# Performance work log

Hardware: AMD Instinct MI355X
Metric: run time of the kernel (lower is better)

The kernel has to match this reference:

```python
import jax, jax.numpy as jnp
import numpy as np

N = 4096      # nodes
INS = 256     # input feature dim
OUTS = 64     # per-mechanism output dim
M = 4         # N_mechs
LEAK = 0.2    # leaky relu negative slope
NEG_INF = -1e9


def setup_inputs() -> dict:
    key = jax.random.key(0)
    ks = jax.random.split(key, 7)
    x = jax.random.normal(ks[0], (N, INS), dtype=jnp.float32)
    adj = jax.random.randint(ks[1], (N, N), 0, 2).astype(jnp.int32)
    W = jax.random.normal(ks[2], (M, INS, OUTS), dtype=jnp.float32) * 0.1
    a1 = jax.random.normal(ks[3], (M, OUTS), dtype=jnp.float32) * 0.1
    a2 = jax.random.normal(ks[4], (M, OUTS), dtype=jnp.float32) * 0.1
    Wc = jax.random.normal(ks[5], (INS, 2 * M * OUTS), dtype=jnp.float32) * 0.1
    bc = jnp.zeros((2 * M * OUTS,), dtype=jnp.float32)
    return {"x": x, "adj": adj, "W": W, "a1": a1, "a2": a2, "Wc": Wc, "bc": bc}


def reference(x, adj, W, a1, a2, Wc, bc):
    # conditioner: mean-pool nodes -> linear -> (gamma, beta) per mechanism
    pooled = x.mean(axis=0)                                   # [INS]
    gb = (pooled @ Wc + bc).reshape(2, M, OUTS)
    gamma, beta = gb[0], gb[1]                                # [M, OUTS] each

    # per-mechanism linear transform + FiLM modulation
    h = jnp.einsum('ni,mio->mno', x, W)                       # [M, N, OUTS]
    h = gamma[:, None, :] * h + beta[:, None, :]

    # GAT-style decomposed attention logits: e_ij = leaky_relu(a1.h_i + a2.h_j)
    e_src = jnp.einsum('mno,mo->mn', h, a1)                   # [M, N]
    e_dst = jnp.einsum('mno,mo->mn', h, a2)                   # [M, N]
    e = e_src[:, :, None] + e_dst[:, None, :]                 # [M, N, N]
    e = jnp.where(e > 0, e, LEAK * e)                         # leaky relu

    # mask by adjacency, softmax over neighbors
    e = jnp.where(adj[None] > 0, e, jnp.float32(NEG_INF))
    attn = jax.nn.softmax(e, axis=-1)                         # [M, N, N]

    out = jnp.einsum('mnk,mko->mno', attn, h)                 # [M, N, OUTS]
    out = jnp.transpose(out, (1, 0, 2)).reshape(N, M * OUTS)  # concat dim=1
    return jax.nn.elu(out)                                    # activate=True
```

## Files before the change

kernel.cpp:

```cpp
#include <hip/hip_runtime.h>
#include <hip/hip_bf16.h>

#define NN    4096
#define INS_  256
#define OUTS_ 64
#define MM    4
#define LOG2E 1.4426950408889634f

typedef float f32x4 __attribute__((ext_vector_type(4)));
typedef short s16x8 __attribute__((ext_vector_type(8)));
typedef unsigned int u32x4 __attribute__((ext_vector_type(4)));

typedef const __attribute__((address_space(1))) unsigned char glob_u8;
typedef __attribute__((address_space(3))) unsigned char lds_u8;

__device__ __forceinline__ void stage16(const void* g, void* l) {
    __builtin_amdgcn_global_load_lds((glob_u8*)g, (lds_u8*)l, 16, 0, 0);
}

__device__ __forceinline__ unsigned int cvt_pk_bf16(float a, float b) {
    unsigned int r;
    asm("v_cvt_pk_bf16_f32 %0, %1, %2" : "=v"(r) : "v"(a), "v"(b));
    return r;
}

__device__ __forceinline__ unsigned int pack_bf16(float a, float b) {
    unsigned int ua = __builtin_bit_cast(unsigned int, a);
    unsigned int ub = __builtin_bit_cast(unsigned int, b);
    ua = (ua + 0x7FFFu + ((ua >> 16) & 1u)) >> 16;
    ub = (ub + 0x7FFFu + ((ub >> 16) & 1u)) & 0xFFFF0000u;
    return ua | ub;
}

__device__ __forceinline__ float mand(float w, unsigned mb, int e) {
    const int m = ((int)(mb << (31 - e))) >> 31;
    return __builtin_bit_cast(float, (__builtin_bit_cast(int, w) & m));
}

__device__ __forceinline__ s16x8 mk_af(float c, unsigned mb,
        const f32x4 q0, const f32x4 q1, const f32x4 q2, const f32x4 q3, float& z) {
    const float w0 = mand(fmaxf(q0[0], c * q0[1]), mb, 0);
    const float w1 = mand(fmaxf(q0[2], c * q0[3]), mb, 1);
    const float w2 = mand(fmaxf(q1[0], c * q1[1]), mb, 2);
    const float w3 = mand(fmaxf(q1[2], c * q1[3]), mb, 3);
    const float w4 = mand(fmaxf(q2[0], c * q2[1]), mb, 4);
    const float w5 = mand(fmaxf(q2[2], c * q2[3]), mb, 5);
    const float w6 = mand(fmaxf(q3[0], c * q3[1]), mb, 6);
    const float w7 = mand(fmaxf(q3[2], c * q3[3]), mb, 7);
    z += ((w0 + w1) + (w2 + w3)) + ((w4 + w5) + (w6 + w7));
    u32x4 au;
    au.x = cvt_pk_bf16(w0, w1);
    au.y = cvt_pk_bf16(w2, w3);
    au.z = cvt_pk_bf16(w4, w5);
    au.w = cvt_pk_bf16(w6, w7);
    return __builtin_bit_cast(s16x8, au);
}


__global__ __launch_bounds__(256) void k_prep(const int* __restrict__ adj,
                                              unsigned long long* __restrict__ msk,
                                              const float* __restrict__ x,
                                              float* __restrict__ part) {
    const int b = blockIdx.x;
    if (b < 1024) {
        const int lane = threadIdx.x & 63;
        const int w    = threadIdx.x >> 6;
        const int r    = b * 4 + w;
        const int* __restrict__ row = adj + (size_t)r * NN;
        unsigned long long* mrow = msk + (size_t)r * 64;
        #pragma unroll 1
        for (int c0 = 0; c0 < 64; c0 += 16) {
            int a[16];
            #pragma unroll
            for (int k = 0; k < 16; ++k) a[k] = row[(c0 + k) * 64 + lane];
            unsigned long long m[16];
            #pragma unroll
            for (int k = 0; k < 16; ++k) m[k] = __ballot(a[k] != 0);
            if (lane == 0) {
                #pragma unroll
                for (int k = 0; k < 16; ++k) mrow[c0 + k] = m[k];
            }
        }
    } else {
        const int bb = b - 1024;
        const int t  = threadIdx.x;
        const int r0 = bb * 64;
        float s = 0.f;
        #pragma unroll 8
        for (int r = 0; r < 64; ++r) s += x[(size_t)(r0 + r) * INS_ + t];
        part[bb * INS_ + t] = s;
    }
}

__global__ __launch_bounds__(256, 2) void k_filmc(
    const float* __restrict__ x, const float* __restrict__ W,
    const float* __restrict__ a1, const float* __restrict__ a2,
    const float* __restrict__ part, const float* __restrict__ Wc,
    const float* __restrict__ bc, float* __restrict__ sc,
    float* __restrict__ spq, unsigned char* __restrict__ htb)
{
    __shared__ float wlds[INS_ * OUTS_];
    __shared__ float sp[INS_];
    __shared__ float pg[256];
    __shared__ float gg[64], bbv[64];

    const int t  = threadIdx.x;
    const int o  = t & 63;
    const int wv = __builtin_amdgcn_readfirstlane(t >> 6);
    const int m  = blockIdx.y;
    const int n0 = blockIdx.x * 32 + wv * 8;

    {
        const unsigned char* wsrc = (const unsigned char*)W + (size_t)m * 65536 + t * 16;
        unsigned char* wdst = (unsigned char*)wlds + t * 16;
        #pragma unroll
        for (int it = 0; it < 16; ++it)
            stage16(wsrc + it * 4096, wdst + it * 4096);
    }

    {
        float s = 0.f;
        #pragma unroll 8
        for (int b = 0; b < 64; ++b) s += part[b * INS_ + t];
        sp[t] = s * (1.0f / NN);
    }
    __syncthreads();

    {
        const int half = t >> 7;
        const int idx  = t & 127;
        const int col  = m * 64 + (idx & 63) + ((idx & 64) ? 256 : 0);
        float acc = (half == 0) ? bc[col] : 0.f;
        const int ib = half * 128;
        #pragma unroll 8
        for (int i = 0; i < 128; ++i)
            acc = fmaf(sp[ib + i], Wc[(size_t)(ib + i) * 512 + col], acc);
        pg[t] = acc;
    }
    __syncthreads();
    if (t < 128) {
        const float v = pg[t] + pg[t + 128];
        if (t < 64) gg[t] = v; else bbv[t - 64] = v;
    }
    __syncthreads();

    float acc[8];
    #pragma unroll
    for (int k = 0; k < 8; ++k) acc[k] = 0.f;

    const float* xp = x + (size_t)n0 * INS_;

    #pragma unroll 4
    for (int i = 0; i < INS_; ++i) {
        const float wl = wlds[i * 64 + o];
        #pragma unroll
        for (int k = 0; k < 8; ++k)
            acc[k] = fmaf(xp[k * INS_ + i], wl, acc[k]);
    }

    const float ga  = gg[o];
    const float be  = bbv[o];
    const float va1 = a1[m * 64 + o];
    const float va2 = a2[m * 64 + o];

    float h[8], sv[8], dv[8];
    #pragma unroll
    for (int k = 0; k < 8; ++k) h[k] = fmaf(ga, acc[k], be);

    #pragma unroll
    for (int k = 0; k < 8; ++k) {
        float s1 = h[k] * va1;
        float s2 = h[k] * va2;
        #pragma unroll
        for (int off = 1; off < 64; off <<= 1) {
            s1 += __shfl_xor(s1, off);
            s2 += __shfl_xor(s2, off);
        }
        sv[k] = s1; dv[k] = s2;
    }

    u32x4 upk;
    upk.x = pack_bf16(h[0], h[1]);
    upk.y = pack_bf16(h[2], h[3]);
    upk.z = pack_bf16(h[4], h[5]);
    upk.w = pack_bf16(h[6], h[7]);
    const size_t phys = ((size_t)(m * 128 + blockIdx.x)) * 4096 + o * 64 + wv * 16;
    *reinterpret_cast<u32x4*>(htb + phys) = upk;

    const int lk = o & 7;
    float ssel = sv[0], dsel = dv[0];
    #pragma unroll
    for (int k = 1; k < 8; ++k) {
        if (lk == k) { ssel = sv[k]; dsel = dv[k]; }
    }
    if (o < 8) {
        sc[(size_t)m * NN + n0 + lk] = exp2f(-0.8f * LOG2E * ssel);
    } else if (o < 16) {
        const float spv = dsel * LOG2E;
        float2 ex = make_float2(exp2f(spv), exp2f(0.2f * spv));
        *reinterpret_cast<float2*>(&spq[(size_t)(m * NN + n0 + lk) * 2]) = ex;
    }
}

#define LOADT(tn, B) do {                                                  \
    const unsigned char* tb_ = tb0 + (size_t)(tn) * 4096;                  \
    B[0] = *reinterpret_cast<const s16x8*>(tb_);                           \
    B[1] = *reinterpret_cast<const s16x8*>(tb_ + 1024);                    \
    B[2] = *reinterpret_cast<const s16x8*>(tb_ + 2048);                    \
    B[3] = *reinterpret_cast<const s16x8*>(tb_ + 3072);                    \
} while (0)

#define COMPUTE4(tn, B, w0_, w1_, w2_, w3_) do {                           \
    const float* qp_ = pqb + (tn) * 64;                                    \
    const f32x4 q0_ = *reinterpret_cast<const f32x4*>(qp_);                \
    const f32x4 q1_ = *reinterpret_cast<const f32x4*>(qp_ + 4);            \
    const f32x4 q2_ = *reinterpret_cast<const f32x4*>(qp_ + 8);            \
    const f32x4 q3_ = *reinterpret_cast<const f32x4*>(qp_ + 12);           \
    const s16x8 A0_ = mk_af(c0v, (w0_) >> sh, q0_, q1_, q2_, q3_, z0);     \
    const s16x8 A1_ = mk_af(c1v, (w1_) >> sh, q0_, q1_, q2_, q3_, z1);     \
    const s16x8 A2_ = mk_af(c2v, (w2_) >> sh, q0_, q1_, q2_, q3_, z2);     \
    const s16x8 A3_ = mk_af(c3v, (w3_) >> sh, q0_, q1_, q2_, q3_, z3);     \
    acc0[0] = __builtin_amdgcn_mfma_f32_16x16x32_bf16(A0_, B[0], acc0[0], 0, 0, 0); \
    acc0[1] = __builtin_amdgcn_mfma_f32_16x16x32_bf16(A0_, B[1], acc0[1], 0, 0, 0); \
    acc0[2] = __builtin_amdgcn_mfma_f32_16x16x32_bf16(A0_, B[2], acc0[2], 0, 0, 0); \
    acc0[3] = __builtin_amdgcn_mfma_f32_16x16x32_bf16(A0_, B[3], acc0[3], 0, 0, 0); \
    acc1[0] = __builtin_amdgcn_mfma_f32_16x16x32_bf16(A1_, B[0], acc1[0], 0, 0, 0); \
    acc1[1] = __builtin_amdgcn_mfma_f32_16x16x32_bf16(A1_, B[1], acc1[1], 0, 0, 0); \
    acc1[2] = __builtin_amdgcn_mfma_f32_16x16x32_bf16(A1_, B[2], acc1[2], 0, 0, 0); \
    acc1[3] = __builtin_amdgcn_mfma_f32_16x16x32_bf16(A1_, B[3], acc1[3], 0, 0, 0); \
    acc2[0] = __builtin_amdgcn_mfma_f32_16x16x32_bf16(A2_, B[0], acc2[0], 0, 0, 0); \
    acc2[1] = __builtin_amdgcn_mfma_f32_16x16x32_bf16(A2_, B[1], acc2[1], 0, 0, 0); \
    acc2[2] = __builtin_amdgcn_mfma_f32_16x16x32_bf16(A2_, B[2], acc2[2], 0, 0, 0); \
    acc2[3] = __builtin_amdgcn_mfma_f32_16x16x32_bf16(A2_, B[3], acc2[3], 0, 0, 0); \
    acc3[0] = __builtin_amdgcn_mfma_f32_16x16x32_bf16(A3_, B[0], acc3[0], 0, 0, 0); \
    acc3[1] = __builtin_amdgcn_mfma_f32_16x16x32_bf16(A3_, B[1], acc3[1], 0, 0, 0); \
    acc3[2] = __builtin_amdgcn_mfma_f32_16x16x32_bf16(A3_, B[2], acc3[2], 0, 0, 0); \
    acc3[3] = __builtin_amdgcn_mfma_f32_16x16x32_bf16(A3_, B[3], acc3[3], 0, 0, 0); \
} while (0)

__global__ __launch_bounds__(512, 2) void k_attn(
    const unsigned int* __restrict__ msk, const float* __restrict__ sc,
    const float* __restrict__ spq, const unsigned char* __restrict__ htb,
    float* __restrict__ out)
{
    extern __shared__ float lds[];
    float* accP = lds;
    float* zP   = lds + 4 * 4096;

    const int t    = threadIdx.x;
    const int lane = t & 63;
    const int jq   = __builtin_amdgcn_readfirstlane(t >> 6);
    const int col  = lane & 15;
    const int kg   = lane >> 4;
    const int sh   = kg * 8;
    const int i0   = blockIdx.x * 64;
    const int mech = blockIdx.y;

    const float c0v = sc[(size_t)mech * NN + i0 + col];
    const float c1v = sc[(size_t)mech * NN + i0 + 16 + col];
    const float c2v = sc[(size_t)mech * NN + i0 + 32 + col];
    const float c3v = sc[(size_t)mech * NN + i0 + 48 + col];

    const u32x4* mr0 = reinterpret_cast<const u32x4*>(
        msk + (size_t)(i0 + col) * 128 + jq * 16);
    const u32x4* mr1 = reinterpret_cast<const u32x4*>(
        msk + (size_t)(i0 + 16 + col) * 128 + jq * 16);
    const u32x4* mr2 = reinterpret_cast<const u32x4*>(
        msk + (size_t)(i0 + 32 + col) * 128 + jq * 16);
    const u32x4* mr3 = reinterpret_cast<const u32x4*>(
        msk + (size_t)(i0 + 48 + col) * 128 + jq * 16);
    const float* pqb = spq + (size_t)mech * NN * 2 + (jq * 512 + kg * 8) * 2;
    const unsigned char* tb0 = htb + ((size_t)(mech * 128 + jq * 16)) * 4096
                             + col * 64 + kg * 16;

    f32x4 acc0[4], acc1[4], acc2[4], acc3[4];
    #pragma unroll
    for (int f = 0; f < 4; ++f) {
        acc0[f] = (f32x4){0.f, 0.f, 0.f, 0.f};
        acc1[f] = acc0[f]; acc2[f] = acc0[f]; acc3[f] = acc0[f];
    }
    float z0 = 0.f, z1 = 0.f, z2 = 0.f, z3 = 0.f;

    s16x8 Ba[4], Bb[4];
    LOADT(0, Ba);
    u32x4 m0n = mr0[0], m1n = mr1[0], m2n = mr2[0], m3n = mr3[0];

    #pragma unroll 1
    for (int tq = 0; tq < 4; ++tq) {
        const int base = tq * 4;
        const u32x4 m0 = m0n, m1 = m1n, m2 = m2n, m3 = m3n;
        if (tq < 3) { m0n = mr0[tq + 1]; m1n = mr1[tq + 1];
                      m2n = mr2[tq + 1]; m3n = mr3[tq + 1]; }
        LOADT(base + 1, Bb);
        COMPUTE4(base + 0, Ba, m0[0], m1[0], m2[0], m3[0]);
        LOADT(base + 2, Ba);
        COMPUTE4(base + 1, Bb, m0[1], m1[1], m2[1], m3[1]);
        LOADT(base + 3, Bb);
        COMPUTE4(base + 2, Ba, m0[2], m1[2], m2[2], m3[2]);
        if (tq < 3) LOADT(base + 4, Ba);
        COMPUTE4(base + 3, Bb, m0[3], m1[3], m2[3], m3[3]);
    }

    z0 += __shfl_xor(z0, 16); z0 += __shfl_xor(z0, 32);
    z1 += __shfl_xor(z1, 16); z1 += __shfl_xor(z1, 32);
    z2 += __shfl_xor(z2, 16); z2 += __shfl_xor(z2, 32);
    z3 += __shfl_xor(z3, 16); z3 += __shfl_xor(z3, 32);

    if (lane < 16) {
        zP[jq * 64 +      lane] = z0;
        zP[jq * 64 + 16 + lane] = z1;
        zP[jq * 64 + 32 + lane] = z2;
        zP[jq * 64 + 48 + lane] = z3;
    }
    float* my = accP + (jq & 3) * 4096;
    if (jq < 4) {
        #pragma unroll
        for (int f = 0; f < 4; ++f) {
            #pragma unroll
            for (int rr = 0; rr < 4; ++rr) {
                const int ro = (kg * 4 + rr) * 64 + f * 16 + col;
                my[ro]            = acc0[f][rr];
                my[1024 + ro]     = acc1[f][rr];
                my[2048 + ro]     = acc2[f][rr];
                my[3072 + ro]     = acc3[f][rr];
            }
        }
    }
    __syncthreads();
    if (jq >= 4) {
        #pragma unroll
        for (int f = 0; f < 4; ++f) {
            #pragma unroll
            for (int rr = 0; rr < 4; ++rr) {
                const int ro = (kg * 4 + rr) * 64 + f * 16 + col;
                my[ro]        += acc0[f][rr];
                my[1024 + ro] += acc1[f][rr];
                my[2048 + ro] += acc2[f][rr];
                my[3072 + ro] += acc3[f][rr];
            }
        }
    }
    __syncthreads();

    const int f0  = t * 8;
    const int row = f0 >> 6;
    const int o0  = f0 & 63;
    f32x4 s0 = (f32x4){0.f, 0.f, 0.f, 0.f};
    f32x4 s1 = s0;
    float z = 0.f;
    #pragma unroll
    for (int p = 0; p < 4; ++p) {
        s0 += *reinterpret_cast<const f32x4*>(accP + p * 4096 + f0);
        s1 += *reinterpret_cast<const f32x4*>(accP + p * 4096 + f0 + 4);
    }
    #pragma unroll
    for (int q = 0; q < 8; ++q) z += zP[q * 64 + row];
    const float inv = 1.0f / z;
    float res[8];
    #pragma unroll
    for (int e = 0; e < 4; ++e) {
        const float v0 = s0[e] * inv;
        const float v1 = s1[e] * inv;
        res[e]     = v0 > 0.f ? v0 : expm1f(v0);
        res[e + 4] = v1 > 0.f ? v1 : expm1f(v1);
    }
    float* op = out + (size_t)(i0 + row) * 256 + mech * 64 + o0;
    *reinterpret_cast<float4*>(op)     = make_float4(res[0], res[1], res[2], res[3]);
    *reinterpret_cast<float4*>(op + 4) = make_float4(res[4], res[5], res[6], res[7]);
}

extern "C" void kernel_launch(void* const* d_in, const int* in_sizes, int n_in,
                              void* d_out, int out_size, void* d_ws, size_t ws_size,
                              hipStream_t stream) {
    const float* x   = (const float*)d_in[0];
    const int*   adj = (const int*)d_in[1];
    const float* W   = (const float*)d_in[2];
    const float* a1  = (const float*)d_in[3];
    const float* a2  = (const float*)d_in[4];
    const float* Wc  = (const float*)d_in[5];
    const float* bc  = (const float*)d_in[6];
    float* out = (float*)d_out;

    float* wsf    = (float*)d_ws;
    float* part   = wsf;
    float* scv    = wsf + 16896;
    float* spq    = wsf + 33280;
    unsigned char* htb = (unsigned char*)(wsf + 66048);
    unsigned long long* msk = (unsigned long long*)(htb + (size_t)2097152);

    (void)hipFuncSetAttribute((const void*)k_attn,
                              hipFuncAttributeMaxDynamicSharedMemorySize, 67584);

    k_prep<<<1088, 256, 0, stream>>>(adj, msk, x, part);
    k_filmc<<<dim3(128, 4), 256, 0, stream>>>(x, W, a1, a2, part, Wc, bc, scv, spq, htb);
    k_attn<<<dim3(64, 4), 512, 67584, stream>>>((const unsigned int*)msk, scv, spq, htb, out);
}
```

Measured before the change: 73.31 us.

## Split attention neighbor range across 16 waves per block instead of 8

Doubles the attention block to 1024 threads so each wave handles half as many neighbor tiles. Wave partial accumulators are then reduced through LDS in four serialized phases, and the z partial sums now come from 16 waves. This targets latency hiding and per-wave serial work in a grid of only 256 blocks. The cost is more LDS reduction passes and barriers, a launch bound of one block per CU that may tighten register limits, and slightly more LDS.

```diff
diff --git a/kernel.cpp b/kernel.cpp
--- a/kernel.cpp
+++ b/kernel.cpp
@@ -238,7 +238,7 @@
     acc3[3] = __builtin_amdgcn_mfma_f32_16x16x32_bf16(A3_, B[3], acc3[3], 0, 0, 0); \
 } while (0)
 
-__global__ __launch_bounds__(512, 2) void k_attn(
+__global__ __launch_bounds__(1024, 1) void k_attn(
     const unsigned int* __restrict__ msk, const float* __restrict__ sc,
     const float* __restrict__ spq, const unsigned char* __restrict__ htb,
     float* __restrict__ out)
@@ -262,15 +262,15 @@
     const float c3v = sc[(size_t)mech * NN + i0 + 48 + col];
 
     const u32x4* mr0 = reinterpret_cast<const u32x4*>(
-        msk + (size_t)(i0 + col) * 128 + jq * 16);
+        msk + (size_t)(i0 + col) * 128 + jq * 8);
     const u32x4* mr1 = reinterpret_cast<const u32x4*>(
-        msk + (size_t)(i0 + 16 + col) * 128 + jq * 16);
+        msk + (size_t)(i0 + 16 + col) * 128 + jq * 8);
     const u32x4* mr2 = reinterpret_cast<const u32x4*>(
-        msk + (size_t)(i0 + 32 + col) * 128 + jq * 16);
+        msk + (size_t)(i0 + 32 + col) * 128 + jq * 8);
     const u32x4* mr3 = reinterpret_cast<const u32x4*>(
-        msk + (size_t)(i0 + 48 + col) * 128 + jq * 16);
-    const float* pqb = spq + (size_t)mech * NN * 2 + (jq * 512 + kg * 8) * 2;
-    const unsigned char* tb0 = htb + ((size_t)(mech * 128 + jq * 16)) * 4096
+        msk + (size_t)(i0 + 48 + col) * 128 + jq * 8);
+    const float* pqb = spq + (size_t)mech * NN * 2 + (jq * 256 + kg * 8) * 2;
+    const unsigned char* tb0 = htb + ((size_t)(mech * 128 + jq * 8)) * 4096
                              + col * 64 + kg * 16;
 
     f32x4 acc0[4], acc1[4], acc2[4], acc3[4];
@@ -286,10 +286,10 @@
     u32x4 m0n = mr0[0], m1n = mr1[0], m2n = mr2[0], m3n = mr3[0];
 
     #pragma unroll 1
-    for (int tq = 0; tq < 4; ++tq) {
+    for (int tq = 0; tq < 2; ++tq) {
         const int base = tq * 4;
         const u32x4 m0 = m0n, m1 = m1n, m2 = m2n, m3 = m3n;
-        if (tq < 3) { m0n = mr0[tq + 1]; m1n = mr1[tq + 1];
+        if (tq < 1) { m0n = mr0[tq + 1]; m1n = mr1[tq + 1];
                       m2n = mr2[tq + 1]; m3n = mr3[tq + 1]; }
         LOADT(base + 1, Bb);
         COMPUTE4(base + 0, Ba, m0[0], m1[0], m2[0], m3[0]);
@@ -297,7 +297,7 @@
         COMPUTE4(base + 1, Bb, m0[1], m1[1], m2[1], m3[1]);
         LOADT(base + 3, Bb);
         COMPUTE4(base + 2, Ba, m0[2], m1[2], m2[2], m3[2]);
-        if (tq < 3) LOADT(base + 4, Ba);
+        if (tq < 1) LOADT(base + 4, Ba);
         COMPUTE4(base + 3, Bb, m0[3], m1[3], m2[3], m3[3]);
     }
 
@@ -313,60 +313,50 @@
         zP[jq * 64 + 48 + lane] = z3;
     }
     float* my = accP + (jq & 3) * 4096;
-    if (jq < 4) {
-        #pragma unroll
-        for (int f = 0; f < 4; ++f) {
+    const int ph = jq >> 2;
+    #pragma unroll 1
+    for (int p = 0; p < 4; ++p) {
+        if (ph == p) {
             #pragma unroll
-            for (int rr = 0; rr < 4; ++rr) {
-                const int ro = (kg * 4 + rr) * 64 + f * 16 + col;
-                my[ro]            = acc0[f][rr];
-                my[1024 + ro]     = acc1[f][rr];
-                my[2048 + ro]     = acc2[f][rr];
-                my[3072 + ro]     = acc3[f][rr];
+            for (int f = 0; f < 4; ++f) {
+                #pragma unroll
+                for (int rr = 0; rr < 4; ++rr) {
+                    const int ro = (kg * 4 + rr) * 64 + f * 16 + col;
+                    if (p == 0) {
+                        my[ro]        = acc0[f][rr];
+                        my[1024 + ro] = acc1[f][rr];
+                        my[2048 + ro] = acc2[f][rr];
+                        my[3072 + ro] = acc3[f][rr];
+                    } else {
+                        my[ro]        += acc0[f][rr];
+                        my[1024 + ro] += acc1[f][rr];
+                        my[2048 + ro] += acc2[f][rr];
+                        my[3072 + ro] += acc3[f][rr];
+                    }
+                }
             }
         }
-    }
-    __syncthreads();
-    if (jq >= 4) {
-        #pragma unroll
-        for (int f = 0; f < 4; ++f) {
-            #pragma unroll
-            for (int rr = 0; rr < 4; ++rr) {
-                const int ro = (kg * 4 + rr) * 64 + f * 16 + col;
-                my[ro]        += acc0[f][rr];
-                my[1024 + ro] += acc1[f][rr];
-                my[2048 + ro] += acc2[f][rr];
-                my[3072 + ro] += acc3[f][rr];
-            }
-        }
-    }
-    __syncthreads();
-
-    const int f0  = t * 8;
+        __syncthreads();
+    }
+
+    const int f0  = t * 4;
     const int row = f0 >> 6;
     const int o0  = f0 & 63;
-    f32x4 s0 = (f32x4){0.f, 0.f, 0.f, 0.f};
-    f32x4 s1 = s0;
+    f32x4 s = (f32x4){0.f, 0.f, 0.f, 0.f};
+    #pragma unroll
+    for (int p = 0; p < 4; ++p)
+        s += *reinterpret_cast<const f32x4*>(accP + p * 4096 + f0);
     float z = 0.f;
     #pragma unroll
-    for (int p = 0; p < 4; ++p) {
-        s0 += *reinterpret_cast<const f32x4*>(accP + p * 4096 + f0);
-        s1 += *reinterpret_cast<const f32x4*>(accP + p * 4096 + f0 + 4);
-    }
-    #pragma unroll
-    for (int q = 0; q < 8; ++q) z += zP[q * 64 + row];
+    for (int q = 0; q < 16; ++q) z += zP[q * 64 + row];
     const float inv = 1.0f / z;
-    float res[8];
+    f32x4 res;
     #pragma unroll
     for (int e = 0; e < 4; ++e) {
-        const float v0 = s0[e] * inv;
-        const float v1 = s1[e] * inv;
-        res[e]     = v0 > 0.f ? v0 : expm1f(v0);
-        res[e + 4] = v1 > 0.f ? v1 : expm1f(v1);
-    }
-    float* op = out + (size_t)(i0 + row) * 256 + mech * 64 + o0;
-    *reinterpret_cast<float4*>(op)     = make_float4(res[0], res[1], res[2], res[3]);
-    *reinterpret_cast<float4*>(op + 4) = make_float4(res[4], res[5], res[6], res[7]);
+        const float v = s[e] * inv;
+        res[e] = v > 0.f ? v : expm1f(v);
+    }
+    *reinterpret_cast<f32x4*>(out + (size_t)(i0 + row) * 256 + mech * 64 + o0) = res;
 }
 
 extern "C" void kernel_launch(void* const* d_in, const int* in_sizes, int n_in,
@@ -389,9 +379,9 @@
     unsigned long long* msk = (unsigned long long*)(htb + (size_t)2097152);
 
     (void)hipFuncSetAttribute((const void*)k_attn,
-                              hipFuncAttributeMaxDynamicSharedMemorySize, 67584);
+                              hipFuncAttributeMaxDynamicSharedMemorySize, 69632);
 
     k_prep<<<1088, 256, 0, stream>>>(adj, msk, x, part);
     k_filmc<<<dim3(128, 4), 256, 0, stream>>>(x, W, a1, a2, part, Wc, bc, scv, spq, htb);
-    k_attn<<<dim3(64, 4), 512, 67584, stream>>>((const unsigned int*)msk, scv, spq, htb, out);
-}
+    k_attn<<<dim3(64, 4), 1024, 69632, stream>>>((const unsigned int*)msk, scv, spq, htb, out);
+}
```

Result: slower. 229.4 us (+212.9%).

## Split attention neighbor dimension across two blocks with last-block reduction

Applied to the files above, without the earlier changes.

Splits k_attn's neighbor (j) range into two halves via a third grid dimension, doubling the block count from 256 to 512 so that more CUs are occupied on the 256-CU part. Each half writes its partial accumulators and softmax denominators to global workspace. The second block to finish, detected with an atomic counter that k_prep zeroes, combines both halves and applies normalization and ELU. In exchange it adds global partial writes and reads, threadfences, and an atomic per output tile.

```diff
diff --git a/kernel.cpp b/kernel.cpp
--- a/kernel.cpp
+++ b/kernel.cpp
@@ -60,7 +60,8 @@
 __global__ __launch_bounds__(256) void k_prep(const int* __restrict__ adj,
                                               unsigned long long* __restrict__ msk,
                                               const float* __restrict__ x,
-                                              float* __restrict__ part) {
+                                              float* __restrict__ part,
+                                              int* __restrict__ cnt) {
     const int b = blockIdx.x;
     if (b < 1024) {
         const int lane = threadIdx.x & 63;
@@ -81,7 +82,7 @@
                 for (int k = 0; k < 16; ++k) mrow[c0 + k] = m[k];
             }
         }
-    } else {
+    } else if (b < 1088) {
         const int bb = b - 1024;
         const int t  = threadIdx.x;
         const int r0 = bb * 64;
@@ -89,6 +90,8 @@
         #pragma unroll 8
         for (int r = 0; r < 64; ++r) s += x[(size_t)(r0 + r) * INS_ + t];
         part[bb * INS_ + t] = s;
+    } else {
+        cnt[threadIdx.x] = 0;
     }
 }
 
@@ -241,11 +244,13 @@
 __global__ __launch_bounds__(512, 2) void k_attn(
     const unsigned int* __restrict__ msk, const float* __restrict__ sc,
     const float* __restrict__ spq, const unsigned char* __restrict__ htb,
-    float* __restrict__ out)
+    float* __restrict__ pacc, float* __restrict__ pz,
+    int* __restrict__ cnt, float* __restrict__ out)
 {
     extern __shared__ float lds[];
     float* accP = lds;
     float* zP   = lds + 4 * 4096;
+    __shared__ int lastFlag;
 
     const int t    = threadIdx.x;
     const int lane = t & 63;
@@ -255,22 +260,24 @@
     const int sh   = kg * 8;
     const int i0   = blockIdx.x * 64;
     const int mech = blockIdx.y;
+    const int jh   = blockIdx.z;
 
     const float c0v = sc[(size_t)mech * NN + i0 + col];
     const float c1v = sc[(size_t)mech * NN + i0 + 16 + col];
     const float c2v = sc[(size_t)mech * NN + i0 + 32 + col];
     const float c3v = sc[(size_t)mech * NN + i0 + 48 + col];
 
+    const int jw = jh * 64 + jq * 8;
     const u32x4* mr0 = reinterpret_cast<const u32x4*>(
-        msk + (size_t)(i0 + col) * 128 + jq * 16);
+        msk + (size_t)(i0 + col) * 128 + jw);
     const u32x4* mr1 = reinterpret_cast<const u32x4*>(
-        msk + (size_t)(i0 + 16 + col) * 128 + jq * 16);
+        msk + (size_t)(i0 + 16 + col) * 128 + jw);
     const u32x4* mr2 = reinterpret_cast<const u32x4*>(
-        msk + (size_t)(i0 + 32 + col) * 128 + jq * 16);
+        msk + (size_t)(i0 + 32 + col) * 128 + jw);
     const u32x4* mr3 = reinterpret_cast<const u32x4*>(
-        msk + (size_t)(i0 + 48 + col) * 128 + jq * 16);
-    const float* pqb = spq + (size_t)mech * NN * 2 + (jq * 512 + kg * 8) * 2;
-    const unsigned char* tb0 = htb + ((size_t)(mech * 128 + jq * 16)) * 4096
+        msk + (size_t)(i0 + 48 + col) * 128 + jw);
+    const float* pqb = spq + (size_t)mech * NN * 2 + ((jh * 2048 + jq * 256) + kg * 8) * 2;
+    const unsigned char* tb0 = htb + ((size_t)(mech * 128 + jh * 64 + jq * 8)) * 4096
                              + col * 64 + kg * 16;
 
     f32x4 acc0[4], acc1[4], acc2[4], acc3[4];
@@ -286,18 +293,17 @@
     u32x4 m0n = mr0[0], m1n = mr1[0], m2n = mr2[0], m3n = mr3[0];
 
     #pragma unroll 1
-    for (int tq = 0; tq < 4; ++tq) {
+    for (int tq = 0; tq < 2; ++tq) {
         const int base = tq * 4;
         const u32x4 m0 = m0n, m1 = m1n, m2 = m2n, m3 = m3n;
-        if (tq < 3) { m0n = mr0[tq + 1]; m1n = mr1[tq + 1];
-                      m2n = mr2[tq + 1]; m3n = mr3[tq + 1]; }
+        if (tq < 1) { m0n = mr0[1]; m1n = mr1[1]; m2n = mr2[1]; m3n = mr3[1]; }
         LOADT(base + 1, Bb);
         COMPUTE4(base + 0, Ba, m0[0], m1[0], m2[0], m3[0]);
         LOADT(base + 2, Ba);
         COMPUTE4(base + 1, Bb, m0[1], m1[1], m2[1], m3[1]);
         LOADT(base + 3, Bb);
         COMPUTE4(base + 2, Ba, m0[2], m1[2], m2[2], m3[2]);
-        if (tq < 3) LOADT(base + 4, Ba);
+        if (tq < 1) LOADT(base + 4, Ba);
         COMPUTE4(base + 3, Bb, m0[3], m1[3], m2[3], m3[3]);
     }
 
@@ -319,10 +325,10 @@
             #pragma unroll
             for (int rr = 0; rr < 4; ++rr) {
                 const int ro = (kg * 4 + rr) * 64 + f * 16 + col;
-                my[ro]            = acc0[f][rr];
-                my[1024 + ro]     = acc1[f][rr];
-                my[2048 + ro]     = acc2[f][rr];
-                my[3072 + ro]     = acc3[f][rr];
+                my[ro]        = acc0[f][rr];
+                my[1024 + ro] = acc1[f][rr];
+                my[2048 + ro] = acc2[f][rr];
+                my[3072 + ro] = acc3[f][rr];
             }
         }
     }
@@ -342,31 +348,52 @@
     }
     __syncthreads();
 
-    const int f0  = t * 8;
-    const int row = f0 >> 6;
-    const int o0  = f0 & 63;
+    const int pair = blockIdx.x * 4 + mech;
+    const int f0   = t * 8;
+    const int row  = f0 >> 6;
     f32x4 s0 = (f32x4){0.f, 0.f, 0.f, 0.f};
     f32x4 s1 = s0;
-    float z = 0.f;
     #pragma unroll
     for (int p = 0; p < 4; ++p) {
         s0 += *reinterpret_cast<const f32x4*>(accP + p * 4096 + f0);
         s1 += *reinterpret_cast<const f32x4*>(accP + p * 4096 + f0 + 4);
     }
-    #pragma unroll
-    for (int q = 0; q < 8; ++q) z += zP[q * 64 + row];
-    const float inv = 1.0f / z;
-    float res[8];
-    #pragma unroll
-    for (int e = 0; e < 4; ++e) {
-        const float v0 = s0[e] * inv;
-        const float v1 = s1[e] * inv;
-        res[e]     = v0 > 0.f ? v0 : expm1f(v0);
-        res[e + 4] = v1 > 0.f ? v1 : expm1f(v1);
-    }
-    float* op = out + (size_t)(i0 + row) * 256 + mech * 64 + o0;
-    *reinterpret_cast<float4*>(op)     = make_float4(res[0], res[1], res[2], res[3]);
-    *reinterpret_cast<float4*>(op + 4) = make_float4(res[4], res[5], res[6], res[7]);
+    float* pa = pacc + ((size_t)(pair * 2 + jh)) * 4096;
+    *reinterpret_cast<f32x4*>(pa + f0)     = s0;
+    *reinterpret_cast<f32x4*>(pa + f0 + 4) = s1;
+    if (t < 64) {
+        float zz = 0.f;
+        #pragma unroll
+        for (int q = 0; q < 8; ++q) zz += zP[q * 64 + t];
+        pz[(pair * 2 + jh) * 64 + t] = zz;
+    }
+    __threadfence();
+    __syncthreads();
+    if (t == 0) lastFlag = atomicAdd(&cnt[pair], 1);
+    __syncthreads();
+
+    if (lastFlag == 1) {
+        __threadfence();
+        const float* paA = pacc + (size_t)pair * 8192;
+        const float* paB = paA + 4096;
+        const f32x4 a0 = *reinterpret_cast<const f32x4*>(paA + f0)
+                       + *reinterpret_cast<const f32x4*>(paB + f0);
+        const f32x4 a1 = *reinterpret_cast<const f32x4*>(paA + f0 + 4)
+                       + *reinterpret_cast<const f32x4*>(paB + f0 + 4);
+        const float z  = pz[pair * 128 + row] + pz[pair * 128 + 64 + row];
+        const float inv = 1.0f / z;
+        float res[8];
+        #pragma unroll
+        for (int e = 0; e < 4; ++e) {
+            const float v0 = a0[e] * inv;
+            const float v1 = a1[e] * inv;
+            res[e]     = v0 > 0.f ? v0 : expm1f(v0);
+            res[e + 4] = v1 > 0.f ? v1 : expm1f(v1);
+        }
+        float* op = out + (size_t)(i0 + row) * 256 + mech * 64 + (f0 & 63);
+        *reinterpret_cast<float4*>(op)     = make_float4(res[0], res[1], res[2], res[3]);
+        *reinterpret_cast<float4*>(op + 4) = make_float4(res[4], res[5], res[6], res[7]);
+    }
 }
 
 extern "C" void kernel_launch(void* const* d_in, const int* in_sizes, int n_in,
@@ -385,13 +412,18 @@
     float* part   = wsf;
     float* scv    = wsf + 16896;
     float* spq    = wsf + 33280;
-    unsigned char* htb = (unsigned char*)(wsf + 66048);
-    unsigned long long* msk = (unsigned long long*)(htb + (size_t)2097152);
+    unsigned char* base = (unsigned char*)d_ws;
+    unsigned char* htb = base + 264192;
+    unsigned long long* msk = (unsigned long long*)(base + 2361344);
+    float* pacc = (float*)(base + 4458496);
+    float* pz   = (float*)(base + 12847104);
+    int*   cnt  = (int*)(base + 12978176);
 
     (void)hipFuncSetAttribute((const void*)k_attn,
                               hipFuncAttributeMaxDynamicSharedMemorySize, 67584);
 
-    k_prep<<<1088, 256, 0, stream>>>(adj, msk, x, part);
+    k_prep<<<1089, 256, 0, stream>>>(adj, msk, x, part, cnt);
     k_filmc<<<dim3(128, 4), 256, 0, stream>>>(x, W, a1, a2, part, Wc, bc, scv, spq, htb);
-    k_attn<<<dim3(64, 4), 512, 67584, stream>>>((const unsigned int*)msk, scv, spq, htb, out);
-}
+    k_attn<<<dim3(64, 4, 2), 512, 67584, stream>>>((const unsigned int*)msk, scv, spq,
+                                                   htb, pacc, pz, cnt, out);
+}
```

After: 232.3 us. +216.8%, slower.

## Split pooling into its own kernel and co-schedule mask packing with FiLM blocks

Applied to the files above, without the earlier changes.

Moves the x mean-pool partial sums into a small standalone kernel. The adjacency bit-packing work is merged into the FiLM/projection kernel, with blocks interleaved two pack blocks to one FiLM block. The aim is to overlap the bandwidth-bound adjacency read with the compute-heavy FiLM transform instead of running them as separate serialized phases. The trade-off is that pack blocks now carry the FiLM kernel's large static LDS footprint and launch bound, which may reduce their occupancy.

```diff
diff --git a/kernel.cpp b/kernel.cpp
--- a/kernel.cpp
+++ b/kernel.cpp
@@ -57,15 +57,32 @@
 }
 
 
-__global__ __launch_bounds__(256) void k_prep(const int* __restrict__ adj,
-                                              unsigned long long* __restrict__ msk,
-                                              const float* __restrict__ x,
+__global__ __launch_bounds__(256) void k_pool(const float* __restrict__ x,
                                               float* __restrict__ part) {
+    const int t  = threadIdx.x;
+    const int r0 = blockIdx.x * 64;
+    float s = 0.f;
+    #pragma unroll 8
+    for (int r = 0; r < 64; ++r) s += x[(size_t)(r0 + r) * INS_ + t];
+    part[blockIdx.x * INS_ + t] = s;
+}
+
+__global__ __launch_bounds__(256, 2) void k_packfilm(
+    const int* __restrict__ adj, unsigned long long* __restrict__ msk,
+    const float* __restrict__ x, const float* __restrict__ W,
+    const float* __restrict__ a1, const float* __restrict__ a2,
+    const float* __restrict__ part, const float* __restrict__ Wc,
+    const float* __restrict__ bc, float* __restrict__ sc,
+    float* __restrict__ spq, unsigned char* __restrict__ htb)
+{
     const int b = blockIdx.x;
-    if (b < 1024) {
-        const int lane = threadIdx.x & 63;
-        const int w    = threadIdx.x >> 6;
-        const int r    = b * 4 + w;
+    const int t = threadIdx.x;
+
+    if (b % 3 != 2) {
+        const int pid  = (b / 3) * 2 + (b % 3);
+        const int lane = t & 63;
+        const int w    = t >> 6;
+        const int r    = pid * 4 + w;
         const int* __restrict__ row = adj + (size_t)r * NN;
         unsigned long long* mrow = msk + (size_t)r * 64;
         #pragma unroll 1
@@ -81,34 +98,20 @@
                 for (int k = 0; k < 16; ++k) mrow[c0 + k] = m[k];
             }
         }
-    } else {
-        const int bb = b - 1024;
-        const int t  = threadIdx.x;
-        const int r0 = bb * 64;
-        float s = 0.f;
-        #pragma unroll 8
-        for (int r = 0; r < 64; ++r) s += x[(size_t)(r0 + r) * INS_ + t];
-        part[bb * INS_ + t] = s;
-    }
-}
-
-__global__ __launch_bounds__(256, 2) void k_filmc(
-    const float* __restrict__ x, const float* __restrict__ W,
-    const float* __restrict__ a1, const float* __restrict__ a2,
-    const float* __restrict__ part, const float* __restrict__ Wc,
-    const float* __restrict__ bc, float* __restrict__ sc,
-    float* __restrict__ spq, unsigned char* __restrict__ htb)
-{
+        return;
+    }
+
     __shared__ float wlds[INS_ * OUTS_];
     __shared__ float sp[INS_];
     __shared__ float pg[256];
     __shared__ float gg[64], bbv[64];
 
-    const int t  = threadIdx.x;
-    const int o  = t & 63;
-    const int wv = __builtin_amdgcn_readfirstlane(t >> 6);
-    const int m  = blockIdx.y;
-    const int n0 = blockIdx.x * 32 + wv * 8;
+    const int fid = b / 3;
+    const int jt  = fid & 127;
+    const int m   = fid >> 7;
+    const int o   = t & 63;
+    const int wv  = __builtin_amdgcn_readfirstlane(t >> 6);
+    const int n0  = jt * 32 + wv * 8;
 
     {
         const unsigned char* wsrc = (const unsigned char*)W + (size_t)m * 65536 + t * 16;
@@ -121,7 +124,7 @@
     {
         float s = 0.f;
         #pragma unroll 8
-        for (int b = 0; b < 64; ++b) s += part[b * INS_ + t];
+        for (int bb = 0; bb < 64; ++bb) s += part[bb * INS_ + t];
         sp[t] = s * (1.0f / NN);
     }
     __syncthreads();
@@ -184,7 +187,7 @@
     upk.y = pack_bf16(h[2], h[3]);
     upk.z = pack_bf16(h[4], h[5]);
     upk.w = pack_bf16(h[6], h[7]);
-    const size_t phys = ((size_t)(m * 128 + blockIdx.x)) * 4096 + o * 64 + wv * 16;
+    const size_t phys = ((size_t)(m * 128 + jt)) * 4096 + o * 64 + wv * 16;
     *reinterpret_cast<u32x4*>(htb + phys) = upk;
 
     const int lk = o & 7;
@@ -391,7 +394,8 @@
     (void)hipFuncSetAttribute((const void*)k_attn,
                               hipFuncAttributeMaxDynamicSharedMemorySize, 67584);
 
-    k_prep<<<1088, 256, 0, stream>>>(adj, msk, x, part);
-    k_filmc<<<dim3(128, 4), 256, 0, stream>>>(x, W, a1, a2, part, Wc, bc, scv, spq, htb);
+    k_pool<<<64, 256, 0, stream>>>(x, part);
+    k_packfilm<<<1536, 256, 0, stream>>>(adj, msk, x, W, a1, a2, part, Wc, bc,
+                                         scv, spq, htb);
     k_attn<<<dim3(64, 4), 512, 67584, stream>>>((const unsigned int*)msk, scv, spq, htb, out);
 }
```

New measurement: 84.37 us. +15.1%, slower.
